# Kernel tuning notes

Hardware: AMD Instinct MI355X
Metric: run time of the kernel (lower is better)

## Reference

```python
import jax, jax.numpy as jnp
import numpy as np

HIDDEN = 1152
NUM_HEADS = 16
HEAD_DIM = HIDDEN // NUM_HEADS  # 72
SEQ = 4096


def rotate_half(x):
    x1 = x[..., : x.shape[-1] // 2]
    x2 = x[..., x.shape[-1] // 2 :]
    return jnp.concatenate((-x2, x1), axis=-1)


def setup_inputs() -> dict:
    key = jax.random.key(0)
    ks = jax.random.split(key, 8)
    hidden_states = jax.random.normal(ks[0], (SEQ, HIDDEN), dtype=jnp.float32)
    cu_seqlens = jnp.sort(jax.random.randint(ks[1], (3,), 0, SEQ)).astype(jnp.int32)
    # rotary embeddings: realistic cos/sin tables
    pos = jnp.arange(SEQ, dtype=jnp.float32)[:, None]
    inv_freq = 1.0 / (10000.0 ** (jnp.arange(0, HEAD_DIM, 2, dtype=jnp.float32) / HEAD_DIM))
    freqs = pos * inv_freq[None, :]  # (SEQ, HEAD_DIM//2)
    emb = jnp.concatenate([freqs, freqs], axis=-1)  # (SEQ, HEAD_DIM)
    cos = jnp.cos(emb)
    sin = jnp.sin(emb)
    std = 0.02
    Wqkv = jax.random.normal(ks[2], (HIDDEN, 3 * HIDDEN), dtype=jnp.float32) * std
    bqkv = jnp.zeros((3 * HIDDEN,), dtype=jnp.float32)
    Wproj = jax.random.normal(ks[3], (HIDDEN, HIDDEN), dtype=jnp.float32) * std
    bproj = jnp.zeros((HIDDEN,), dtype=jnp.float32)
    return {
        "hidden_states": hidden_states,
        "cu_seqlens": cu_seqlens,
        "cos": cos,
        "sin": sin,
        "Wqkv": Wqkv,
        "bqkv": bqkv,
        "Wproj": Wproj,
        "bproj": bproj,
    }


def reference(hidden_states, cu_seqlens, cos, sin, Wqkv, bqkv, Wproj, bproj):
    seq_len = hidden_states.shape[0]
    scale = HEAD_DIM ** -0.5
    qkv = hidden_states @ Wqkv + bqkv  # (S, 3*H)
    qkv = qkv.reshape(seq_len, 3, NUM_HEADS, HEAD_DIM).transpose(1, 0, 2, 3)
    q, k, v = qkv[0], qkv[1], qkv[2]  # each (S, nH, hd)
    # inline RoPE in fp32
    orig_dtype = q.dtype
    qf = q.astype(jnp.float32)
    kf = k.astype(jnp.float32)
    c = cos[:, None, :].astype(jnp.float32)
    s = sin[:, None, :].astype(jnp.float32)
    q = (qf * c + rotate_half(qf) * s).astype(orig_dtype)
    k = (kf * c + rotate_half(kf) * s).astype(orig_dtype)
    # (nH, S, hd)
    q = q.transpose(1, 0, 2)
    k = k.transpose(1, 0, 2)
    v = v.transpose(1, 0, 2)
    attn = jnp.einsum('hqd,hkd->hqk', q, k) * scale
    attn = jax.nn.softmax(attn, axis=-1)
    out = jnp.einsum('hqk,hkd->hqd', attn, v)  # (nH, S, hd)
    out = out.transpose(1, 0, 2).reshape(seq_len, HIDDEN)
    return out @ Wproj + bproj
```

## Files before the change

### kernel.cpp

```cpp
#include <hip/hip_runtime.h>
#include <hip/hip_bf16.h>
#include <stdint.h>

#define SEQ 4096
#define HID 1152
#define NH  16
#define HD  72
#define N3  3456
#define DQ  80
#define QBLK 256
#define TILE_B 19584
#define TILE_E 9792
#define VBASE 10240
#define ZOFF  58752

typedef __bf16 bf16;
typedef __bf16 bf16x8 __attribute__((ext_vector_type(8)));
typedef float  f32x4  __attribute__((ext_vector_type(4)));
typedef float  f32x16 __attribute__((ext_vector_type(16)));
typedef uint32_t u32x4 __attribute__((ext_vector_type(4)));

#define EXP2F(x) __builtin_amdgcn_exp2f(x)
#define PLSWAP(a, b) asm("v_permlane32_swap_b32 %0, %1" : "+v"(a), "+v"(b))

__device__ __forceinline__ void gload_lds16(const void* g, void* l) {
    __builtin_amdgcn_global_load_lds(
        (__attribute__((address_space(1))) void*)(void*)g,
        (__attribute__((address_space(3))) void*)l, 16, 0, 0);
}
__device__ __forceinline__ uint16_t bfbits(float x) {
    return __builtin_bit_cast(uint16_t, (bf16)x);
}

__global__ __launch_bounds__(256)
void prep(const float* __restrict__ hidden, const float* __restrict__ Wqkv,
          const float* __restrict__ Wproj, bf16* __restrict__ hid_b,
          bf16* __restrict__ WqkvT, bf16* __restrict__ WprojT)
{
    __shared__ float tl[32][33];
    int b = blockIdx.x, tid = threadIdx.x;
    if (b < 2304) {
        int i = b * 256 + tid;
        const float4* p = (const float4*)hidden + (size_t)i * 2;
        float4 a = p[0], c = p[1];
        bf16x8 o;
        o[0]=(bf16)a.x; o[1]=(bf16)a.y; o[2]=(bf16)a.z; o[3]=(bf16)a.w;
        o[4]=(bf16)c.x; o[5]=(bf16)c.y; o[6]=(bf16)c.z; o[7]=(bf16)c.w;
        ((bf16x8*)hid_b)[i] = o;
        return;
    }
    const float* in; bf16* out; int R, C, c0, r0;
    if (b < 6192) {
        int bb = b - 2304;
        in = Wqkv; out = WqkvT; R = HID; C = N3;
        c0 = (bb % 108) * 32; r0 = (bb / 108) * 32;
    } else {
        int bb = b - 6192;
        in = Wproj; out = WprojT; R = HID; C = HID;
        c0 = (bb % 36) * 32; r0 = (bb / 36) * 32;
    }
    int tx = tid & 31, ty = tid >> 5;
#pragma unroll
    for (int i = 0; i < 4; ++i)
        tl[ty + 8*i][tx] = in[(size_t)(r0 + ty + 8*i) * C + c0 + tx];
    __syncthreads();
#pragma unroll
    for (int i = 0; i < 4; ++i)
        out[(size_t)(c0 + ty + 8*i) * R + r0 + tx] = (bf16)tl[tx][ty + 8*i];
}

template<int OUT_F32>
__global__ __launch_bounds__(256)
void gemm_bt(const bf16* __restrict__ A, const bf16* __restrict__ BT,
             const float* __restrict__ bias, void* __restrict__ out,
             int M, int N, int K)
{
    __shared__ __align__(16) bf16 As[128 * 64];
    __shared__ __align__(16) bf16 Bs[128 * 64];
    int tid = threadIdx.x;
    int lane = tid & 63, w = tid >> 6;
    int wm = w & 1, wn = w >> 1;
    int orig = blockIdx.y * gridDim.x + blockIdx.x;
    int xcd = orig & 7, v = orig >> 3;
    int mpx = gridDim.x >> 3;
    int m0 = (xcd * mpx + (v % mpx)) * 128;
    int n0 = (v / mpx) * 128;
    int lq = lane & 15, lk = lane >> 4;

    int kx0 = ((lk ^ (lq & 7)) << 4);
    int kx1 = (((4 + lk) ^ (lq & 7)) << 4);

    f32x4 acc[4][4] = {};

    for (int k0 = 0; k0 < K; k0 += 64) {
        __syncthreads();
#pragma unroll
        for (int j = 0; j < 4; ++j) {
            int c = j * 256 + tid;
            int row = c >> 3, kc = c & 7;
            int koff = k0 + ((kc ^ (row & 7)) << 3);
            gload_lds16(A  + (size_t)(m0 + row) * K + koff, (char*)As + c * 16);
            gload_lds16(BT + (size_t)(n0 + row) * K + koff, (char*)Bs + c * 16);
        }
        __syncthreads();
#pragma unroll
        for (int ks = 0; ks < 2; ++ks) {
            int kx = ks ? kx1 : kx0;
            bf16x8 af[4], bfr[4];
#pragma unroll
            for (int m = 0; m < 4; ++m)
                af[m] = *(const bf16x8*)((char*)As + (wm * 64 + m * 16 + lq) * 128 + kx);
#pragma unroll
            for (int n = 0; n < 4; ++n)
                bfr[n] = *(const bf16x8*)((char*)Bs + (wn * 64 + n * 16 + lq) * 128 + kx);
#pragma unroll
            for (int m = 0; m < 4; ++m)
#pragma unroll
                for (int n = 0; n < 4; ++n)
                    acc[m][n] = __builtin_amdgcn_mfma_f32_16x16x32_bf16(af[m], bfr[n], acc[m][n], 0, 0, 0);
        }
    }

    int rb = m0 + wm * 64, cb = n0 + wn * 64;
#pragma unroll
    for (int m = 0; m < 4; ++m) {
#pragma unroll
        for (int n = 0; n < 4; ++n) {
            int col = cb + n * 16 + lq;
            float b = bias[col];
#pragma unroll
            for (int r = 0; r < 4; ++r) {
                int row = rb + m * 16 + lk * 4 + r;
                float v2 = acc[m][n][r] + b;
                if (OUT_F32) ((float*)out)[(size_t)row * N + col] = v2;
                else         ((bf16*)out)[(size_t)row * N + col] = (bf16)v2;
            }
        }
    }
}

__global__ __launch_bounds__(256)
void pack(const bf16* __restrict__ qkv, const float* __restrict__ cs,
          const float* __restrict__ sn, bf16* __restrict__ Qp,
          bf16* __restrict__ KVp)
{
    __shared__ __align__(16) bf16 tl[64][80];
    int b = blockIdx.x, tid = threadIdx.x;
    if (b < 20480) {
        int idx = b * 256 + tid;
        int dd = idx % 80;
        int rest = idx / 80;
        int s = rest & (SEQ - 1), h = rest >> 12;
        float qv = 0.f, kv = 0.f;
        if (dd < HD) {
            const bf16* row = qkv + (size_t)s * N3 + h * HD;
            float c  = cs[s * HD + dd], si = sn[s * HD + dd];
            int   dp = (dd < 36) ? dd + 36 : dd - 36;
            float sg = (dd < 36) ? -1.f : 1.f;
            float qa = (float)row[dd],       qb = (float)row[dp];
            float ka = (float)row[HID + dd], kb = (float)row[HID + dp];
            qv = (qa * c + sg * qb * si) * (0.11785113019775793f * 1.4426950408889634f);
            kv =  ka * c + sg * kb * si;
        }
        int t = s >> 6, key = s & 63;
        int dchunk = dd >> 3;
        int pos = (dchunk < 8) ? (dchunk ^ (key & 7)) : dchunk;
        KVp[((size_t)(h * 64 + t)) * TILE_E + key * 80 + pos * 8 + (dd & 7)] = (bf16)kv;
        Qp[((size_t)h * SEQ + s) * DQ + dd] = (bf16)qv;
        return;
    }
    int bb = b - 20480;
    int t = bb & 63, h = bb >> 6, s0 = t * 64;
    for (int i = tid; i < 64 * 9; i += 256) {
        int key = i / 9, c8 = (i % 9) * 8;
        *(bf16x8*)&tl[key][c8] =
            *(const bf16x8*)&qkv[(size_t)(s0 + key) * N3 + 2 * HID + h * HD + c8];
    }
    __syncthreads();
    bf16* dst = KVp + ((size_t)(h * 64 + t)) * TILE_E + 5120;
    for (int vcid = tid; vcid < 584; vcid += 256) {
        int d = vcid >> 3, cpos = vcid & 7;
        int kb8 = (cpos ^ (d & 7)) << 3;
        bf16x8 v;
#pragma unroll
        for (int j = 0; j < 8; ++j)
            v[j] = (d < HD) ? tl[kb8 + j][d] : (bf16)1.f;
        *(bf16x8*)&dst[vcid * 8] = v;
    }
}

__global__ __launch_bounds__(512, 2)
void attn_fwd13(const bf16* __restrict__ Qp, const bf16* __restrict__ KVp,
                bf16* __restrict__ Oout)
{
    __shared__ __align__(16) char smem[59392];

    const int o = blockIdx.x;
    const int x = o & 7, s = o >> 3;
    const int h  = x * 2 + (s >> 4);
    const int q0 = (s & 15) * QBLK;
    const int tid = threadIdx.x, lane = tid & 63, w = tid >> 6;
    const int ql = lane & 31, hi = lane >> 5;
    const int q  = q0 + w * 32 + ql;

    bf16x8 qf[5];
    const bf16* qbase = Qp + ((size_t)h * SEQ + q) * DQ + hi * 8;
#pragma unroll
    for (int ks = 0; ks < 5; ++ks) qf[ks] = *(const bf16x8*)(qbase + ks * 16);

    int aK[5];
#pragma unroll
    for (int ks = 0; ks < 4; ++ks)
        aK[ks] = ql * 160 + (((ks * 2 + hi) ^ (ql & 7)) * 16);
    aK[4] = ql * 160 + (8 + hi) * 16;
    int aV[4];
#pragma unroll
    for (int u = 0; u < 4; ++u)
        aV[u] = VBASE + ql * 128 + (((u * 2 + hi) ^ (ql & 7)) * 16);

    f32x16 o_[3] = {};

    const bf16* kvh = KVp + (size_t)h * (64 * TILE_E);

#define STAGE(T, DB) do {                                                      \
        const bf16* s_ = kvh + (size_t)(T) * TILE_E;                           \
        _Pragma("unroll")                                                      \
        for (int j_ = 0; j_ < 3; ++j_) {                                       \
            int c_ = j_ * 512 + tid;                                           \
            if (c_ < 1224) gload_lds16(s_ + c_ * 8, smem + (DB) + c_ * 16);    \
        }                                                                      \
    } while (0)

    auto qk = [&](const char* bK, f32x16& sa, f32x16& sb) {
        __builtin_amdgcn_s_setprio(1);
#pragma unroll
        for (int ks = 0; ks < 5; ++ks) {
            bf16x8 kf = *(const bf16x8*)(bK + aK[ks]);
            sa = __builtin_amdgcn_mfma_f32_32x32x16_bf16(kf, qf[ks], sa, 0, 0, 0);
        }
#pragma unroll
        for (int ks = 0; ks < 5; ++ks) {
            bf16x8 kf = *(const bf16x8*)(bK + 5120 + aK[ks]);
            sb = __builtin_amdgcn_mfma_f32_32x32x16_bf16(kf, qf[ks], sb, 0, 0, 0);
        }
        __builtin_amdgcn_s_setprio(0);
    };

    auto expv = [&](const f32x16& sa, const f32x16& sb, const char* bV) {
        uint32_t wd[16];
#pragma unroll
        for (int i = 0; i < 8; ++i) {
            wd[i]   = (uint32_t)bfbits(EXP2F(sa[2*i])) | ((uint32_t)bfbits(EXP2F(sa[2*i+1])) << 16);
            wd[8+i] = (uint32_t)bfbits(EXP2F(sb[2*i])) | ((uint32_t)bfbits(EXP2F(sb[2*i+1])) << 16);
        }
        PLSWAP(wd[0], wd[2]);   PLSWAP(wd[1], wd[3]);
        PLSWAP(wd[4], wd[6]);   PLSWAP(wd[5], wd[7]);
        PLSWAP(wd[8], wd[10]);  PLSWAP(wd[9], wd[11]);
        PLSWAP(wd[12], wd[14]); PLSWAP(wd[13], wd[15]);
        u32x4 u0 = {wd[0],wd[1],wd[2],wd[3]},   u1 = {wd[4],wd[5],wd[6],wd[7]};
        u32x4 u2 = {wd[8],wd[9],wd[10],wd[11]}, u3 = {wd[12],wd[13],wd[14],wd[15]};
        bf16x8 pb[4] = { __builtin_bit_cast(bf16x8, u0), __builtin_bit_cast(bf16x8, u1),
                         __builtin_bit_cast(bf16x8, u2), __builtin_bit_cast(bf16x8, u3) };
        __builtin_amdgcn_s_setprio(1);
#pragma unroll
        for (int db = 0; db < 3; ++db)
#pragma unroll
            for (int u = 0; u < 4; ++u) {
                const char* pv;
                if (db < 2)          pv = bV + db * 4096 + aV[u];
                else if (ql <= 8)    pv = bV + 8192 + aV[u];
                else                 pv = smem + ZOFF;
                bf16x8 vf = *(const bf16x8*)pv;
                o_[db] = __builtin_amdgcn_mfma_f32_32x32x16_bf16(vf, pb[u], o_[db], 0, 0, 0);
            }
        __builtin_amdgcn_s_setprio(0);
    };

    f32x16 pa = {}, pb_ = {};

    if (tid < 4) ((float*)(smem + ZOFF))[tid] = 0.f;
    STAGE(0, 0);
    asm volatile("s_waitcnt vmcnt(0) lgkmcnt(0)" ::: "memory");
    __builtin_amdgcn_s_barrier();
    STAGE(1, TILE_B);
    qk(smem, pa, pb_);
    asm volatile("s_waitcnt vmcnt(0)" ::: "memory");
    __builtin_amdgcn_s_barrier();

#define BODY(T, KB, VB, SB) do {                                               \
        if ((T) < 63) STAGE((T) + 1, SB);                                      \
        f32x16 ca = {}, cb = {};                                               \
        qk(smem + (KB), ca, cb);                                               \
        expv(pa, pb_, smem + (VB));                                            \
        pa = ca; pb_ = cb;                                                     \
        __builtin_amdgcn_sched_barrier(0);                                     \
        asm volatile("s_waitcnt vmcnt(0)" ::: "memory");                       \
        __builtin_amdgcn_s_barrier();                                          \
    } while (0)

    for (int t = 1; t < 64; t += 3) {
        BODY(t,     TILE_B,     0,          2 * TILE_B);
        BODY(t + 1, 2 * TILE_B, TILE_B,     0);
        BODY(t + 2, 0,          2 * TILE_B, TILE_B);
    }
    expv(pa, pb_, smem);
#undef BODY
#undef STAGE

    __syncthreads();
    bf16* Os = (bf16*)smem;
    {
        float lv  = o_[2][4];
        float lo_ = __shfl_xor(lv, 32);
        float invl = 1.0f / (hi ? lo_ : lv);
        int qloc = w * 32 + ql;
#pragma unroll
        for (int db = 0; db < 3; ++db)
#pragma unroll
            for (int r = 0; r < 16; ++r) {
                int dloc = (r & 3) + 8 * (r >> 2) + 4 * hi;
                int d = db * 32 + dloc;
                if (d < HD) Os[qloc * 82 + d] = (bf16)(o_[db][r] * invl);
            }
    }
    __syncthreads();
    for (int i = tid; i < QBLK * 36; i += 512) {
        int row = i / 36, c = i % 36;
        uint32_t val = *(const uint32_t*)((const char*)Os + row * 164 + c * 4);
        *(uint32_t*)((char*)Oout + (size_t)(q0 + row) * 2304 + h * 144 + c * 4) = val;
    }
}

extern "C" void kernel_launch(void* const* d_in, const int* in_sizes, int n_in,
                              void* d_out, int out_size, void* d_ws, size_t ws_size,
                              hipStream_t stream)
{
    const float* hidden = (const float*)d_in[0];
    const float* cosT  = (const float*)d_in[2];
    const float* sinT  = (const float*)d_in[3];
    const float* Wqkv  = (const float*)d_in[4];
    const float* bqkv  = (const float*)d_in[5];
    const float* Wproj = (const float*)d_in[6];
    const float* bproj = (const float*)d_in[7];

    char* ws = (char*)d_ws;
    size_t off = 0;
    auto alloc = [&](size_t bytes) {
        char* p = ws + off;
        off += (bytes + 255) & ~(size_t)255;
        return p;
    };
    bf16* hid_b  = (bf16*)alloc((size_t)SEQ * HID * 2);
    bf16* WqkvT  = (bf16*)alloc((size_t)N3  * HID * 2);
    bf16* WprojT = (bf16*)alloc((size_t)HID * HID * 2);
    bf16* qkv_b  = (bf16*)alloc((size_t)SEQ * N3  * 2);
    bf16* Qp     = (bf16*)alloc((size_t)NH * SEQ * DQ * 2);
    bf16* KVp    = (bf16*)alloc((size_t)NH * 64 * TILE_E * 2);
    bf16* attno  = hid_b;

    prep<<<7488, 256, 0, stream>>>(hidden, Wqkv, Wproj, hid_b, WqkvT, WprojT);
    gemm_bt<0><<<dim3(SEQ / 128, N3 / 128), 256, 0, stream>>>(hid_b, WqkvT, bqkv, qkv_b,
                                                              SEQ, N3, HID);
    pack<<<21504, 256, 0, stream>>>(qkv_b, cosT, sinT, Qp, KVp);
    attn_fwd13<<<dim3(SEQ / QBLK * NH), 512, 0, stream>>>(Qp, KVp, attno);
    gemm_bt<1><<<dim3(SEQ / 128, HID / 128), 256, 0, stream>>>(attno, WprojT, bproj, d_out,
                                                               SEQ, HID, HID);
}
```

Measured before the change: 197.8 us.

## Widen K tile rows to 128 with 16-way swizzle; vectorize weight transpose

```diff
diff --git a/kernel.cpp b/kernel.cpp
--- a/kernel.cpp
+++ b/kernel.cpp
@@ -9,12 +9,13 @@
 #define N3  3456
 #define DQ  80
 #define QBLK 256
-#define TILE_B 19584
-#define TILE_E 9792
-#define VBASE 10240
-#define ZOFF  58752
+#define TILE_B 25728
+#define TILE_E 12864
+#define VBASE 16384
+#define ZOFF  77184
 
 typedef __bf16 bf16;
+typedef __bf16 bf16x4 __attribute__((ext_vector_type(4)));
 typedef __bf16 bf16x8 __attribute__((ext_vector_type(8)));
 typedef float  f32x4  __attribute__((ext_vector_type(4)));
 typedef float  f32x16 __attribute__((ext_vector_type(16)));
@@ -37,7 +38,7 @@
           const float* __restrict__ Wproj, bf16* __restrict__ hid_b,
           bf16* __restrict__ WqkvT, bf16* __restrict__ WprojT)
 {
-    __shared__ float tl[32][33];
+    __shared__ float tl[32][136];
     int b = blockIdx.x, tid = threadIdx.x;
     if (b < 2304) {
         int i = b * 256 + tid;
@@ -50,23 +51,32 @@
         return;
     }
     const float* in; bf16* out; int R, C, c0, r0;
-    if (b < 6192) {
+    if (b < 3276) {
         int bb = b - 2304;
         in = Wqkv; out = WqkvT; R = HID; C = N3;
-        c0 = (bb % 108) * 32; r0 = (bb / 108) * 32;
+        r0 = (bb / 27) * 32; c0 = (bb % 27) * 128;
     } else {
-        int bb = b - 6192;
+        int bb = b - 3276;
         in = Wproj; out = WprojT; R = HID; C = HID;
-        c0 = (bb % 36) * 32; r0 = (bb / 36) * 32;
+        r0 = (bb / 9) * 32; c0 = (bb % 9) * 128;
     }
     int tx = tid & 31, ty = tid >> 5;
 #pragma unroll
-    for (int i = 0; i < 4; ++i)
-        tl[ty + 8*i][tx] = in[(size_t)(r0 + ty + 8*i) * C + c0 + tx];
+    for (int i = 0; i < 4; ++i) {
+        int row = ty + 8 * i;
+        float4 v = *(const float4*)&in[(size_t)(r0 + row) * C + c0 + tx * 4];
+        *(float4*)&tl[row][tx * 4] = v;
+    }
     __syncthreads();
-#pragma unroll
-    for (int i = 0; i < 4; ++i)
-        out[(size_t)(c0 + ty + 8*i) * R + r0 + tx] = (bf16)tl[tx][ty + 8*i];
+    int cb = tid >> 3, r4 = (tid & 7) * 4;
+#pragma unroll
+    for (int cc = 0; cc < 4; ++cc) {
+        int c = cb + cc * 32;
+        bf16x4 o;
+#pragma unroll
+        for (int j = 0; j < 4; ++j) o[j] = (bf16)tl[r4 + j][c];
+        *(bf16x4*)&out[(size_t)(c0 + c) * R + r0 + r4] = o;
+    }
 }
 
 template<int OUT_F32>
@@ -146,11 +156,11 @@
 {
     __shared__ __align__(16) bf16 tl[64][80];
     int b = blockIdx.x, tid = threadIdx.x;
-    if (b < 20480) {
+    if (b < 32768) {
         int idx = b * 256 + tid;
-        int dd = idx % 80;
-        int rest = idx / 80;
-        int s = rest & (SEQ - 1), h = rest >> 12;
+        int dd = idx & 127;
+        int s  = (idx >> 7) & (SEQ - 1);
+        int h  = idx >> 19;
         float qv = 0.f, kv = 0.f;
         if (dd < HD) {
             const bf16* row = qkv + (size_t)s * N3 + h * HD;
@@ -163,13 +173,12 @@
             kv =  ka * c + sg * kb * si;
         }
         int t = s >> 6, key = s & 63;
-        int dchunk = dd >> 3;
-        int pos = (dchunk < 8) ? (dchunk ^ (key & 7)) : dchunk;
-        KVp[((size_t)(h * 64 + t)) * TILE_E + key * 80 + pos * 8 + (dd & 7)] = (bf16)kv;
-        Qp[((size_t)h * SEQ + s) * DQ + dd] = (bf16)qv;
+        int chunk = key * 16 + ((dd >> 3) ^ (key & 15));
+        KVp[((size_t)(h * 64 + t)) * TILE_E + chunk * 8 + (dd & 7)] = (bf16)kv;
+        if (dd < DQ) Qp[((size_t)h * SEQ + s) * DQ + dd] = (bf16)qv;
         return;
     }
-    int bb = b - 20480;
+    int bb = b - 32768;
     int t = bb & 63, h = bb >> 6, s0 = t * 64;
     for (int i = tid; i < 64 * 9; i += 256) {
         int key = i / 9, c8 = (i % 9) * 8;
@@ -177,7 +186,7 @@
             *(const bf16x8*)&qkv[(size_t)(s0 + key) * N3 + 2 * HID + h * HD + c8];
     }
     __syncthreads();
-    bf16* dst = KVp + ((size_t)(h * 64 + t)) * TILE_E + 5120;
+    bf16* dst = KVp + ((size_t)(h * 64 + t)) * TILE_E + 8192;
     for (int vcid = tid; vcid < 584; vcid += 256) {
         int d = vcid >> 3, cpos = vcid & 7;
         int kb8 = (cpos ^ (d & 7)) << 3;
@@ -190,10 +199,10 @@
 }
 
 __global__ __launch_bounds__(512, 2)
-void attn_fwd13(const bf16* __restrict__ Qp, const bf16* __restrict__ KVp,
+void attn_fwd14(const bf16* __restrict__ Qp, const bf16* __restrict__ KVp,
                 bf16* __restrict__ Oout)
 {
-    __shared__ __align__(16) char smem[59392];
+    __shared__ __align__(16) char smem[77312];
 
     const int o = blockIdx.x;
     const int x = o & 7, s = o >> 3;
@@ -210,9 +219,8 @@
 
     int aK[5];
 #pragma unroll
-    for (int ks = 0; ks < 4; ++ks)
-        aK[ks] = ql * 160 + (((ks * 2 + hi) ^ (ql & 7)) * 16);
-    aK[4] = ql * 160 + (8 + hi) * 16;
+    for (int ks = 0; ks < 5; ++ks)
+        aK[ks] = ql * 256 + (((ks * 2 + hi) ^ (ql & 15)) * 16);
     int aV[4];
 #pragma unroll
     for (int u = 0; u < 4; ++u)
@@ -225,9 +233,9 @@
 #define STAGE(T, DB) do {                                                      \
         const bf16* s_ = kvh + (size_t)(T) * TILE_E;                           \
         _Pragma("unroll")                                                      \
-        for (int j_ = 0; j_ < 3; ++j_) {                                       \
+        for (int j_ = 0; j_ < 4; ++j_) {                                       \
             int c_ = j_ * 512 + tid;                                           \
-            if (c_ < 1224) gload_lds16(s_ + c_ * 8, smem + (DB) + c_ * 16);    \
+            if (c_ < 1608) gload_lds16(s_ + c_ * 8, smem + (DB) + c_ * 16);    \
         }                                                                      \
     } while (0)
 
@@ -240,7 +248,7 @@
         }
 #pragma unroll
         for (int ks = 0; ks < 5; ++ks) {
-            bf16x8 kf = *(const bf16x8*)(bK + 5120 + aK[ks]);
+            bf16x8 kf = *(const bf16x8*)(bK + 8192 + aK[ks]);
             sb = __builtin_amdgcn_mfma_f32_32x32x16_bf16(kf, qf[ks], sb, 0, 0, 0);
         }
         __builtin_amdgcn_s_setprio(0);
@@ -358,11 +366,11 @@
     bf16* KVp    = (bf16*)alloc((size_t)NH * 64 * TILE_E * 2);
     bf16* attno  = hid_b;
 
-    prep<<<7488, 256, 0, stream>>>(hidden, Wqkv, Wproj, hid_b, WqkvT, WprojT);
+    prep<<<3600, 256, 0, stream>>>(hidden, Wqkv, Wproj, hid_b, WqkvT, WprojT);
     gemm_bt<0><<<dim3(SEQ / 128, N3 / 128), 256, 0, stream>>>(hid_b, WqkvT, bqkv, qkv_b,
                                                               SEQ, N3, HID);
-    pack<<<21504, 256, 0, stream>>>(qkv_b, cosT, sinT, Qp, KVp);
-    attn_fwd13<<<dim3(SEQ / QBLK * NH), 512, 0, stream>>>(Qp, KVp, attno);
+    pack<<<33792, 256, 0, stream>>>(qkv_b, cosT, sinT, Qp, KVp);
+    attn_fwd14<<<dim3(SEQ / QBLK * NH), 512, 0, stream>>>(Qp, KVp, attno);
     gemm_bt<1><<<dim3(SEQ / 128, HID / 128), 256, 0, stream>>>(attno, WprojT, bproj, d_out,
                                                                SEQ, HID, HID);
 }
```

Result: slower. 202.3 us (+2.2%).
